# Optimization experiments

Hardware: AMD Instinct MI355X
Metric: run time of the kernel (lower is better)

The kernel has to match this reference:

```python
import jax, jax.numpy as jnp
from jax import lax
import numpy as np

DN = ('NCHW', 'OIHW', 'NCHW')

def conv(x, w, b, stride, pad):
    y = lax.conv_general_dilated(x, w, (stride, stride), [(pad, pad), (pad, pad)], dimension_numbers=DN)
    return y + b[None, :, None, None]

def conv_t(x, w, b, stride, pad):
    # PyTorch ConvTranspose2d weight layout is (in, out, kh, kw); flip spatially, swap to OIHW,
    # and realize transpose-conv as lhs-dilated conv with padding k-1-p.
    k = w.shape[2]
    wt = jnp.flip(w, (2, 3)).transpose(1, 0, 2, 3)
    q = k - 1 - pad
    y = lax.conv_general_dilated(x, wt, (1, 1), [(q, q), (q, q)], lhs_dilation=(stride, stride), dimension_numbers=DN)
    return y + b[None, :, None, None]

def setup_inputs() -> dict:
    key = jax.random.key(0)
    ks = jax.random.split(key, 16)
    K, C = 512, 64
    def he(k, shape, fan_in):
        return jax.random.normal(k, shape, jnp.float32) * np.float32(np.sqrt(2.0 / fan_in))
    return {
        'x': jax.random.normal(ks[0], (64, 1, 256, 256), jnp.float32),
        'e1_w': he(ks[1], (32, 1, 4, 4), 1 * 16), 'e1_b': jnp.zeros((32,), jnp.float32),
        'e2_w': he(ks[2], (64, 32, 4, 4), 32 * 16), 'e2_b': jnp.zeros((64,), jnp.float32),
        'e3_w': he(ks[3], (64, 64, 3, 3), 64 * 9), 'e3_b': jnp.zeros((64,), jnp.float32),
        'emb': jax.random.uniform(ks[4], (K, C), jnp.float32, -1.0 / K, 1.0 / K),
        'd1_w': he(ks[5], (64, 32, 3, 3), 64 * 9), 'd1_b': jnp.zeros((32,), jnp.float32),
        'd2_w': he(ks[6], (32, 64, 4, 4), 32 * 16), 'd2_b': jnp.zeros((64,), jnp.float32),
        'd3_w': he(ks[7], (64, 1, 4, 4), 64 * 16), 'd3_b': jnp.zeros((1,), jnp.float32),
    }

def reference(x, e1_w, e1_b, e2_w, e2_b, e3_w, e3_b, emb, d1_w, d1_b, d2_w, d2_b, d3_w, d3_b):
    # encoder
    h = jax.nn.relu(conv(x, e1_w, e1_b, 2, 1))
    h = jax.nn.relu(conv(h, e2_w, e2_b, 2, 1))
    ze = jax.nn.relu(conv(h, e3_w, e3_b, 1, 1))  # (N, C, H, W)
    N, C, H, W = ze.shape
    # VQ: nearest codebook entry per spatial location via ||z||^2 - 2 z.e + ||e||^2
    zf = ze.transpose(0, 2, 3, 1).reshape(-1, C)  # (N*H*W, C)
    dist = (zf * zf).sum(-1, keepdims=True) - 2.0 * (zf @ emb.T) + (emb * emb).sum(-1)[None, :]
    idx = jnp.argmin(dist, axis=1)  # (N*H*W,)
    zq = emb[idx].reshape(N, H, W, C).transpose(0, 3, 1, 2)  # (N, C, H, W)
    # straight-through estimator
    dec_in = ze + lax.stop_gradient(zq - ze)
    # decoder
    h = jax.nn.relu(conv_t(dec_in, d1_w, d1_b, 1, 1))
    h = jax.nn.relu(conv_t(h, d2_w, d2_b, 2, 1))
    x_hat = conv_t(h, d3_w, d3_b, 2, 1)
    return (x_hat, ze, zq)
```

## Files before the change

kernel.cpp:

```cpp
#include <hip/hip_runtime.h>

typedef short short8 __attribute__((ext_vector_type(8)));
typedef float f32x4 __attribute__((ext_vector_type(4)));

union U8 { short8 s8; unsigned int u[4]; };

__device__ __forceinline__ unsigned short f2bf(float f) {
    unsigned int u = __float_as_uint(f);
    u = (u + 0x7fffu + ((u >> 16) & 1u)) >> 16;
    return (unsigned short)u;
}
__device__ __forceinline__ float bf2f(unsigned short s) {
    return __uint_as_float(((unsigned int)s) << 16);
}


__global__ __launch_bounds__(256) void k_e1i(
    const float* __restrict__ x, const float* __restrict__ e1w, const float* __restrict__ e1b,
    unsigned short* __restrict__ h1p2, unsigned int* __restrict__ ws_dw,
    const float* __restrict__ e2w, const float* __restrict__ e3w,
    const float* __restrict__ d1w, const float* __restrict__ d2w,
    const float* __restrict__ d3w, const float* __restrict__ emb,
    unsigned short* __restrict__ ape2, unsigned short* __restrict__ ape3,
    unsigned short* __restrict__ apd1, unsigned short* __restrict__ apd2,
    unsigned short* __restrict__ apd3, unsigned short* __restrict__ embbf,
    float* __restrict__ hninit)
{
    int bid = blockIdx.x;
    if (bid < 4096) {
        int idx = bid * 256 + threadIdx.x;
        int ow = idx & 127, oh = (idx >> 7) & 127, n = idx >> 14;
        const float* xn = x + (size_t)n * 65536;
        float patch[16];
#pragma unroll
        for (int kh = 0; kh < 4; kh++) {
            int ih = 2 * oh + kh - 1;
#pragma unroll
            for (int kw = 0; kw < 4; kw++) {
                int iw = 2 * ow + kw - 1;
                bool ok = ((unsigned)ih < 256u) & ((unsigned)iw < 256u);
                patch[kh * 4 + kw] = ok ? xn[ih * 256 + iw] : 0.f;
            }
        }
        unsigned int outw[16];
#pragma unroll
        for (int oc = 0; oc < 32; oc++) {
            float acc = e1b[oc];
#pragma unroll
            for (int t = 0; t < 16; t++) acc += patch[t] * e1w[oc * 16 + t];
            unsigned short bf = f2bf(fmaxf(acc, 0.f));
            if (oc & 1) outw[oc >> 1] |= ((unsigned int)bf) << 16;
            else        outw[oc >> 1] = bf;
        }
        int par = ow & 1;
        int cidx = (ow + par) >> 1;
        size_t base = ((size_t)((idx >> 14) * 130 + oh + 1) * 2 + par) * 2112 + cidx * 32;
        uint4* dst = (uint4*)(h1p2 + base);
#pragma unroll
        for (int i = 0; i < 4; i++) dst[i] = *(uint4*)&outw[i * 4];
        return;
    }
    if (bid < 11376) {
        int t = (bid - 4096) * 256 + threadIdx.x;
        if (t < 270336) {
            int img = t / 4224, q = t % 4224;
            int rowsel = q / 2112, rem = q % 2112;
            ws_dw[img * 274560 + rowsel * 129 * 2112 + rem] = 0u;
        } else if (t < 532480) {
            int g = t - 270336;
            int img = g / 4096, q = g % 4096;
            int row = 1 + (q >> 5), c2 = q & 31;
            int sel = c2 >> 4, ch = c2 & 15;
            int par = sel ? 0 : 1, idx2 = sel ? 64 : 0;
            ws_dw[img * 274560 + row * 2112 + par * 1056 + idx2 * 16 + ch] = 0u;
        } else if (t < 1863680) {
            unsigned int base, Cd, r;
            if (t < 1064960)      { base = 17571840u; Cd = 32; r = t - 532480;  }
            else if (t < 1597440) { base = 34881536u; Cd = 32; r = t - 1064960; }
            else                  { base = 43802624u; Cd = 16; r = t - 1597440; }
            unsigned int per_img = 260u * Cd;
            unsigned int img = r / per_img, q = r % per_img;
            unsigned int p = q / Cd, c = q % Cd;
            unsigned int row, col;
            if (p < 66u)        { row = 0;  col = p; }
            else if (p < 132u)  { row = 65; col = p - 66u; }
            else { unsigned int s = p - 132u; row = 1 + (s >> 1); col = (s & 1) ? 65u : 0u; }
            ws_dw[base + ((img * 66u + row) * 66u + col) * Cd + c] = 0u;
        }
        return;
    }
    int f = (bid - 11376) * 256 + threadIdx.x;
    if (f < 4096) {
        int ks = f >> 8, mt = (f >> 6) & 3, lane = f & 63;
        int quad = lane >> 4, l16 = lane & 15;
        int oc = mt * 16 + l16, kh = ks >> 2, kw = ks & 3;
        short8 sv;
#pragma unroll
        for (int j = 0; j < 8; j++) {
            int ic = quad * 8 + j;
            sv[j] = (short)f2bf(e2w[((oc * 32 + ic) * 4 + kh) * 4 + kw]);
        }
        ((short8*)ape2)[f] = sv;
    } else if (f < 8704) {
        int g = f - 4096;
        int ks = g >> 8, mt = (g >> 6) & 3, lane = g & 63;
        int quad = lane >> 4, l16 = lane & 15;
        int oc = mt * 16 + l16, tap = ks >> 1, kh = tap / 3, kw = tap % 3;
        int icb = (ks & 1) * 32 + quad * 8;
        short8 sv;
#pragma unroll
        for (int j = 0; j < 8; j++)
            sv[j] = (short)f2bf(e3w[((oc * 64 + icb + j) * 3 + kh) * 3 + kw]);
        ((short8*)ape3)[g] = sv;
    } else if (f < 11008) {
        int g = f - 8704;
        int ks = g >> 7, mt = (g >> 6) & 1, lane = g & 63;
        int quad = lane >> 4, l16 = lane & 15;
        int oc = mt * 16 + l16, tap = ks >> 1, kh = tap / 3, kw = tap % 3;
        int icb = (ks & 1) * 32 + quad * 8;
        short8 sv;
#pragma unroll
        for (int j = 0; j < 8; j++)
            sv[j] = (short)f2bf(d1w[(((icb + j) * 32 + oc) * 3 + (2 - kh)) * 3 + (2 - kw)]);
        ((short8*)apd1)[g] = sv;
    } else if (f < 15104) {
        int g = f - 11008;
        int par = g >> 10, ks = (g >> 8) & 3, mt = (g >> 6) & 3, lane = g & 63;
        int quad = lane >> 4, l16 = lane & 15;
        int ph = par >> 1, pw = par & 1, a = ks >> 1, bb = ks & 1;
        int kh = 3 - ph - 2 * a, kw = 3 - pw - 2 * bb;
        int oc = mt * 16 + l16;
        short8 sv;
#pragma unroll
        for (int j = 0; j < 8; j++) {
            int ic = quad * 8 + j;
            sv[j] = (short)f2bf(d2w[((ic * 64 + oc) * 4 + kh) * 4 + kw]);
        }
        ((short8*)apd2)[g] = sv;
    } else if (f < 15232) {
        int g = f - 15104;
        int ks = g >> 6, lane = g & 63;
        int quad = lane >> 4, tap = lane & 15;
        short8 sv;
#pragma unroll
        for (int j = 0; j < 8; j++) {
            int ic = ks * 32 + quad * 8 + j;
            sv[j] = (short)f2bf(d3w[ic * 16 + tap]);
        }
        ((short8*)apd3)[g] = sv;
    } else if (f < 19328) {
        int g = f - 15232;
        int code = g >> 3, chb = (g & 7) * 8;
        short8 sv;
#pragma unroll
        for (int j = 0; j < 8; j++) sv[j] = (short)f2bf(emb[code * 64 + chb + j]);
        ((short8*)embbf)[g] = sv;
    } else if (f < 19840) {
        int code = f - 19328;
        float s = 0.f;
        for (int c = 0; c < 64; c++) { float v = emb[code * 64 + c]; s += v * v; }
        hninit[code] = 2.0f - 0.5f * s;
    }
}

template<int CIN, int COUT, int KSTEPS, int NCH, int WPIN, int MODE>
__global__ __launch_bounds__(256, 4) void k_conv(const unsigned short* __restrict__ inp,
                                                 const unsigned short* __restrict__ aprep,
                                                 const float* __restrict__ bias,
                                                 unsigned short* __restrict__ out0) {
    constexpr int MT = COUT / 16;
    constexpr int KCH = KSTEPS / NCH;
    __shared__ short8 sA[KCH * MT * 64];
    int tid = threadIdx.x;
    int wave = tid >> 6, lane = tid & 63, quad = lane >> 4, l16 = lane & 15;
    int bid = blockIdx.x;
    int n = bid >> 4, rg = bid & 15;
    int oh = rg * 4 + wave;

    int base0;
    if (MODE == 0) base0 = (n * 130 + 2 * oh) * 4224 + quad * 8;
    else           base0 = n * (WPIN * WPIN * CIN) + ((oh + 1) * WPIN + 1) * CIN + quad * 8;

    f32x4 acc[4][MT];
#pragma unroll
    for (int t = 0; t < 4; t++)
#pragma unroll
        for (int mt = 0; mt < MT; mt++)
            acc[t][mt] = *(const f32x4*)(bias + mt * 16 + quad * 4);

#pragma unroll
    for (int ch = 0; ch < NCH; ch++) {
        for (int i = tid; i < KCH * MT * 64; i += 256)
            sA[i] = ((const short8*)aprep)[ch * (KCH * MT * 64) + i];
        __syncthreads();
#pragma unroll
        for (int k = 0; k < KCH; k++) {
            int ks = ch * KCH + k;
            int off, pxs;
            if (MODE == 0) {
                int kh = ks >> 2, kw = ks & 3;
                int par = (kw & 1) ^ 1;
                off = kh * 4224 + par * 2112 + (kw >> 1) * 32;
                pxs = 32;
            } else {
                int tap = ks >> 1, kh = tap / 3, kw = tap % 3;
                off = ((kh - 1) * WPIN + (kw - 1)) * CIN + (ks & 1) * 32;
                pxs = CIN;
            }
            short8 bfr[4];
#pragma unroll
            for (int t = 0; t < 4; t++)
                bfr[t] = *(const short8*)(inp + base0 + (t * 16 + l16) * pxs + off);
#pragma unroll
            for (int mt = 0; mt < MT; mt++) {
                short8 a = sA[(k * MT + mt) * 64 + lane];
#pragma unroll
                for (int t = 0; t < 4; t++)
                    acc[t][mt] = __builtin_amdgcn_mfma_f32_16x16x32_bf16(a, bfr[t], acc[t][mt], 0, 0, 0);
            }
        }
        if (ch + 1 < NCH) __syncthreads();
    }

#pragma unroll
    for (int t = 0; t < 4; t++) {
        int ow = t * 16 + l16;
#pragma unroll
        for (int mt = 0; mt < MT; mt++) {
            float v0 = fmaxf(acc[t][mt][0], 0.f), v1 = fmaxf(acc[t][mt][1], 0.f);
            float v2 = fmaxf(acc[t][mt][2], 0.f), v3 = fmaxf(acc[t][mt][3], 0.f);
            unsigned int lo = (unsigned int)f2bf(v0) | ((unsigned int)f2bf(v1) << 16);
            unsigned int hi = (unsigned int)f2bf(v2) | ((unsigned int)f2bf(v3) << 16);
            uint2 uu; uu.x = lo; uu.y = hi;
            int oc = mt * 16 + quad * 4;
            if (MODE == 0) {
                size_t addr = (size_t)n * 278784 + ((oh + 1) * 66 + ow + 1) * 64 + oc;
                *(uint2*)(out0 + addr) = uu;
            } else {
                size_t addr = (size_t)n * 139392 + ((oh + 1) * 66 + ow + 1) * 32 + oc;
                *(uint2*)(out0 + addr) = uu;
            }
        }
    }
}

__global__ __launch_bounds__(256, 4) void k_e3vq(const unsigned short* __restrict__ h2p,
                                                 const unsigned short* __restrict__ ape3,
                                                 const float* __restrict__ bias,
                                                 const unsigned short* __restrict__ embbf,
                                                 const float* __restrict__ hninit,
                                                 float* __restrict__ ze_out,
                                                 float* __restrict__ zq_out,
                                                 unsigned short* __restrict__ zqp) {
    __shared__ short8 sA[9 * 4 * 64];
    int tid = threadIdx.x;
    int wave = tid >> 6, lane = tid & 63, quad = lane >> 4, l16 = lane & 15;
    int bid = blockIdx.x;
    int n = bid >> 4, rg = bid & 15;
    int oh = rg * 4 + wave;
    int base0 = n * 278784 + ((oh + 1) * 66 + 1) * 64 + quad * 8;

    f32x4 acc[4][4];
#pragma unroll
    for (int t = 0; t < 4; t++)
#pragma unroll
        for (int mt = 0; mt < 4; mt++)
            acc[t][mt] = *(const f32x4*)(bias + mt * 16 + quad * 4);

#pragma unroll
    for (int ch = 0; ch < 2; ch++) {
        for (int i = tid; i < 9 * 4 * 64; i += 256)
            sA[i] = ((const short8*)ape3)[ch * (9 * 4 * 64) + i];
        __syncthreads();
#pragma unroll
        for (int k = 0; k < 9; k++) {
            int ks = ch * 9 + k;
            int tap = ks >> 1, kh = tap / 3, kw = tap % 3;
            int off = ((kh - 1) * 66 + (kw - 1)) * 64 + (ks & 1) * 32;
            short8 bfr[4];
#pragma unroll
            for (int t = 0; t < 4; t++)
                bfr[t] = *(const short8*)(h2p + base0 + (t * 16 + l16) * 64 + off);
#pragma unroll
            for (int mt = 0; mt < 4; mt++) {
                short8 a = sA[(k * 4 + mt) * 64 + lane];
#pragma unroll
                for (int t = 0; t < 4; t++)
                    acc[t][mt] = __builtin_amdgcn_mfma_f32_16x16x32_bf16(a, bfr[t], acc[t][mt], 0, 0, 0);
            }
        }
        if (ch == 0) __syncthreads();
    }

#pragma unroll
    for (int t = 0; t < 4; t++)
#pragma unroll
        for (int mt = 0; mt < 4; mt++)
#pragma unroll
            for (int r = 0; r < 4; r++)
                acc[t][mt][r] = fmaxf(acc[t][mt][r], 0.f);

#pragma unroll
    for (int t = 0; t < 4; t++) {
        int px = oh * 64 + t * 16 + l16;
#pragma unroll
        for (int mt = 0; mt < 4; mt++) {
            int oc = mt * 16 + quad * 4;
#pragma unroll
            for (int r = 0; r < 4; r++)
                __builtin_nontemporal_store(acc[t][mt][r], &ze_out[((size_t)n * 64 + oc + r) * 4096 + px]);
        }
    }

    short8 b0[4], b1[4];
    int s0 = (((2 * quad) & 3) << 4) | l16;
    int s1 = (((2 * quad + 1) & 3) << 4) | l16;
#pragma unroll
    for (int t = 0; t < 4; t++) {
        f32x4 xv = (quad < 2) ? acc[t][0] : acc[t][1];
        f32x4 yv = (quad < 2) ? acc[t][2] : acc[t][3];
        unsigned int xa = (unsigned int)f2bf(xv[0]) | ((unsigned int)f2bf(xv[1]) << 16);
        unsigned int xb = (unsigned int)f2bf(xv[2]) | ((unsigned int)f2bf(xv[3]) << 16);
        unsigned int ya = (unsigned int)f2bf(yv[0]) | ((unsigned int)f2bf(yv[1]) << 16);
        unsigned int yb = (unsigned int)f2bf(yv[2]) | ((unsigned int)f2bf(yv[3]) << 16);
        U8 ub0, ub1;
        ub0.u[0] = (unsigned int)__shfl((int)xa, s0); ub0.u[1] = (unsigned int)__shfl((int)xb, s0);
        ub0.u[2] = (unsigned int)__shfl((int)xa, s1); ub0.u[3] = (unsigned int)__shfl((int)xb, s1);
        ub1.u[0] = (unsigned int)__shfl((int)ya, s0); ub1.u[1] = (unsigned int)__shfl((int)yb, s0);
        ub1.u[2] = (unsigned int)__shfl((int)ya, s1); ub1.u[3] = (unsigned int)__shfl((int)yb, s1);
        b0[t] = ub0.s8; b1[t] = ub1.s8;
    }

    unsigned int bk[4] = {0u, 0u, 0u, 0u};
#pragma unroll 4
    for (int j0 = 0; j0 < 512; j0 += 16) {
        short8 a0 = *(const short8*)(embbf + (j0 + l16) * 64 + quad * 8);
        short8 a1 = *(const short8*)(embbf + (j0 + l16) * 64 + 32 + quad * 8);
        f32x4 ci = *(const f32x4*)(hninit + j0 + quad * 4);
        int iv = 511 - j0 - quad * 4;
#pragma unroll
        for (int t = 0; t < 4; t++) {
            f32x4 s = __builtin_amdgcn_mfma_f32_16x16x32_bf16(a0, b0[t], ci, 0, 0, 0);
            s = __builtin_amdgcn_mfma_f32_16x16x32_bf16(a1, b1[t], s, 0, 0, 0);
#pragma unroll
            for (int r = 0; r < 4; r++) {
                unsigned int key = (__float_as_uint(s[r]) & 0xFFFFFE00u) | (unsigned int)(iv - r);
                bk[t] = bk[t] > key ? bk[t] : key;
            }
        }
    }
#pragma unroll
    for (int t = 0; t < 4; t++) {
        unsigned int o1 = (unsigned int)__shfl_xor((int)bk[t], 16);
        bk[t] = bk[t] > o1 ? bk[t] : o1;
        unsigned int o2 = (unsigned int)__shfl_xor((int)bk[t], 32);
        bk[t] = bk[t] > o2 ? bk[t] : o2;
    }
#pragma unroll
    for (int t = 0; t < 4; t++) {
        int code = 511 - (int)(bk[t] & 511u);
        int col = t * 16 + l16;
        int hw = oh * 64 + col;
        uint4 u0 = *(const uint4*)(embbf + code * 64 + quad * 16);
        uint4 u1 = *(const uint4*)(embbf + code * 64 + quad * 16 + 8);
        size_t qaddr = (size_t)n * 278784 + ((oh + 1) * 66 + (col + 1)) * 64 + quad * 16;
        *(uint4*)(zqp + qaddr) = u0;
        *(uint4*)(zqp + qaddr + 8) = u1;
        size_t zb = ((size_t)n * 64 + quad * 16) * 4096 + hw;
        unsigned int uw[8] = {u0.x, u0.y, u0.z, u0.w, u1.x, u1.y, u1.z, u1.w};
#pragma unroll
        for (int i = 0; i < 8; i++) {
            __builtin_nontemporal_store(__uint_as_float(uw[i] << 16), &zq_out[zb + (2 * i + 0) * 4096]);
            __builtin_nontemporal_store(__uint_as_float(uw[i] & 0xFFFF0000u), &zq_out[zb + (2 * i + 1) * 4096]);
        }
    }
}

__global__ __launch_bounds__(256, 3) void k_d2f(const unsigned short* __restrict__ d1op,
                                                const unsigned short* __restrict__ apd2,
                                                const float* __restrict__ bias,
                                                const unsigned short* __restrict__ apd3,
                                                unsigned short* __restrict__ sc16) {
    __shared__ short8 sA[1024];
    int tid = threadIdx.x;
    int wave = tid >> 6, lane = tid & 63, quad = lane >> 4, l16 = lane & 15;
    int bid = blockIdx.x;
    int n = bid >> 6, par = (bid >> 4) & 3, rg = bid & 15;
    int oh = rg * 4 + wave;
    int ph = par >> 1, pw = par & 1;

    short8 pa0 = ((const short8*)apd3)[lane];
    short8 pa1 = ((const short8*)apd3)[64 + lane];

    for (int i = tid; i < 1024; i += 256) sA[i] = ((const short8*)apd2)[par * 1024 + i];
    __syncthreads();

    int base0 = n * 139392 + ((oh + ph) * 66 + pw) * 32 + quad * 8;
    f32x4 acc[4][4];
#pragma unroll
    for (int t = 0; t < 4; t++)
#pragma unroll
        for (int mt = 0; mt < 4; mt++)
            acc[t][mt] = *(const f32x4*)(bias + mt * 16 + quad * 4);

#pragma unroll
    for (int k = 0; k < 4; k++) {
        int a_ = k >> 1, bb = k & 1;
        int off = (a_ * 66 + bb) * 32;
        short8 bfr[4];
#pragma unroll
        for (int t = 0; t < 4; t++)
            bfr[t] = *(const short8*)(d1op + base0 + (t * 16 + l16) * 32 + off);
#pragma unroll
        for (int mt = 0; mt < 4; mt++) {
            short8 a = sA[(k * 4 + mt) * 64 + lane];
#pragma unroll
            for (int t = 0; t < 4; t++)
                acc[t][mt] = __builtin_amdgcn_mfma_f32_16x16x32_bf16(a, bfr[t], acc[t][mt], 0, 0, 0);
        }
    }

    int s0 = (((2 * quad) & 3) << 4) | l16;
    int s1 = (((2 * quad + 1) & 3) << 4) | l16;
    int oh_out = 2 * oh + ph;
#pragma unroll
    for (int t = 0; t < 4; t++) {
#pragma unroll
        for (int mt = 0; mt < 4; mt++)
#pragma unroll
            for (int r = 0; r < 4; r++)
                acc[t][mt][r] = fmaxf(acc[t][mt][r], 0.f);
        f32x4 xv = (quad < 2) ? acc[t][0] : acc[t][1];
        f32x4 yv = (quad < 2) ? acc[t][2] : acc[t][3];
        unsigned int xa = (unsigned int)f2bf(xv[0]) | ((unsigned int)f2bf(xv[1]) << 16);
        unsigned int xb = (unsigned int)f2bf(xv[2]) | ((unsigned int)f2bf(xv[3]) << 16);
        unsigned int ya = (unsigned int)f2bf(yv[0]) | ((unsigned int)f2bf(yv[1]) << 16);
        unsigned int yb = (unsigned int)f2bf(yv[2]) | ((unsigned int)f2bf(yv[3]) << 16);
        U8 ub0, ub1;
        ub0.u[0] = (unsigned int)__shfl((int)xa, s0); ub0.u[1] = (unsigned int)__shfl((int)xb, s0);
        ub0.u[2] = (unsigned int)__shfl((int)xa, s1); ub0.u[3] = (unsigned int)__shfl((int)xb, s1);
        ub1.u[0] = (unsigned int)__shfl((int)ya, s0); ub1.u[1] = (unsigned int)__shfl((int)yb, s0);
        ub1.u[2] = (unsigned int)__shfl((int)ya, s1); ub1.u[3] = (unsigned int)__shfl((int)yb, s1);
        f32x4 sc = {0.f, 0.f, 0.f, 0.f};
        sc = __builtin_amdgcn_mfma_f32_16x16x32_bf16(pa0, ub0.s8, sc, 0, 0, 0);
        sc = __builtin_amdgcn_mfma_f32_16x16x32_bf16(pa1, ub1.s8, sc, 0, 0, 0);
        int ow_out = 2 * (t * 16 + l16) + pw;
        int pbaseo = n * 16384 + oh_out * 128 + ow_out;
#pragma unroll
        for (int r = 0; r < 4; r++) {
            int tap = quad * 4 + r;
            sc16[(size_t)tap * 1048576 + pbaseo] = f2bf(sc[r]);
        }
    }
}

__global__ __launch_bounds__(256) void k_d3e(const unsigned short* __restrict__ sc16,
                                             const float* __restrict__ d3b,
                                             float* __restrict__ xhat) {
    int idx = blockIdx.x * 256 + threadIdx.x;
    int ow = idx & 255, oh = (idx >> 8) & 255, n = idx >> 16;
    float acc = d3b[0];
    int kh0 = (oh + 1) & 1, kw0 = (ow + 1) & 1;
#pragma unroll
    for (int dh = 0; dh < 2; dh++) {
        int kh = kh0 + 2 * dh;
        int ih = (oh + 1 - kh) >> 1;
        bool vh = ((unsigned)ih < 128u);
#pragma unroll
        for (int dw = 0; dw < 2; dw++) {
            int kw = kw0 + 2 * dw;
            int iw = (ow + 1 - kw) >> 1;
            if (vh && ((unsigned)iw < 128u))
                acc += bf2f(sc16[(size_t)(kh * 4 + kw) * 1048576 + n * 16384 + ih * 128 + iw]);
        }
    }
    __builtin_nontemporal_store(acc, &xhat[(size_t)n * 65536 + oh * 256 + ow]);
}

extern "C" void kernel_launch(void* const* d_in, const int* in_sizes, int n_in,
                              void* d_out, int out_size, void* d_ws, size_t ws_size,
                              hipStream_t stream) {
    const float* x    = (const float*)d_in[0];
    const float* e1w  = (const float*)d_in[1];
    const float* e1b  = (const float*)d_in[2];
    const float* e2w  = (const float*)d_in[3];
    const float* e2b  = (const float*)d_in[4];
    const float* e3w  = (const float*)d_in[5];
    const float* e3b  = (const float*)d_in[6];
    const float* emb  = (const float*)d_in[7];
    const float* d1w  = (const float*)d_in[8];
    const float* d1b  = (const float*)d_in[9];
    const float* d2w  = (const float*)d_in[10];
    const float* d2b  = (const float*)d_in[11];
    const float* d3w  = (const float*)d_in[12];
    const float* d3b  = (const float*)d_in[13];

    float* xhat = (float*)d_out;
    float* ze   = xhat + 4194304;
    float* zq   = ze + 16777216;

    char* ws = (char*)d_ws;
    unsigned short* h1p2   = (unsigned short*)(ws + 0);
    unsigned short* h2p    = (unsigned short*)(ws + 70287360);
    unsigned short* zqp    = (unsigned short*)(ws + 139526144);
    unsigned short* d1op   = (unsigned short*)(ws + 175210496);
    unsigned short* sc16   = (unsigned short*)(ws + 193052672);
    unsigned short* ape2   = (unsigned short*)(ws + 226607104);
    unsigned short* ape3   = (unsigned short*)(ws + 226672640);
    unsigned short* apd1   = (unsigned short*)(ws + 226746368);
    unsigned short* apd2   = (unsigned short*)(ws + 226783232);
    unsigned short* apd3   = (unsigned short*)(ws + 226848768);
    unsigned short* embbf  = (unsigned short*)(ws + 226850816);
    float*          hninit = (float*)(ws + 226916352);

    k_e1i<<<11454, 256, 0, stream>>>(x, e1w, e1b, h1p2, (unsigned int*)d_ws,
                                     e2w, e3w, d1w, d2w, d3w, emb,
                                     ape2, ape3, apd1, apd2, apd3, embbf, hninit);
    k_conv<32, 64, 16, 2, 0, 0><<<1024, 256, 0, stream>>>(h1p2, ape2, e2b, h2p);
    k_e3vq<<<1024, 256, 0, stream>>>(h2p, ape3, e3b, embbf, hninit, ze, zq, zqp);
    k_conv<64, 32, 18, 2, 66, 2><<<1024, 256, 0, stream>>>(zqp, apd1, d1b, d1op);
    k_d2f<<<4096, 256, 0, stream>>>(d1op, apd2, d2b, apd3, sc16);
    k_d3e<<<16384, 256, 0, stream>>>(sc16, d3b, xhat);
}
```

Measured before the change: 422.9 us.

## Split VQ codebook search across waves via shared-memory tiles and cross-wave argmax

```diff
diff --git a/kernel.cpp b/kernel.cpp
--- a/kernel.cpp
+++ b/kernel.cpp
@@ -252,7 +252,11 @@
                                                  float* __restrict__ ze_out,
                                                  float* __restrict__ zq_out,
                                                  unsigned short* __restrict__ zqp) {
-    __shared__ short8 sA[9 * 4 * 64];
+    __shared__ __align__(16) char smem[36864];
+    short8* sA = (short8*)smem;
+    short8* sB = (short8*)smem;
+    unsigned int* cross = (unsigned int*)(smem + 32768);
+
     int tid = threadIdx.x;
     int wave = tid >> 6, lane = tid & 63, quad = lane >> 4, l16 = lane & 15;
     int bid = blockIdx.x;
@@ -291,6 +295,7 @@
         }
         if (ch == 0) __syncthreads();
     }
+    __syncthreads();
 
 #pragma unroll
     for (int t = 0; t < 4; t++)
@@ -312,7 +317,6 @@
         }
     }
 
-    short8 b0[4], b1[4];
     int s0 = (((2 * quad) & 3) << 4) | l16;
     int s1 = (((2 * quad + 1) & 3) << 4) | l16;
 #pragma unroll
@@ -328,20 +332,28 @@
         ub0.u[2] = (unsigned int)__shfl((int)xa, s1); ub0.u[3] = (unsigned int)__shfl((int)xb, s1);
         ub1.u[0] = (unsigned int)__shfl((int)ya, s0); ub1.u[1] = (unsigned int)__shfl((int)yb, s0);
         ub1.u[2] = (unsigned int)__shfl((int)ya, s1); ub1.u[3] = (unsigned int)__shfl((int)yb, s1);
-        b0[t] = ub0.s8; b1[t] = ub1.s8;
-    }
-
-    unsigned int bk[4] = {0u, 0u, 0u, 0u};
-#pragma unroll 4
-    for (int j0 = 0; j0 < 512; j0 += 16) {
+        sB[(wave * 8 + 2 * t + 0) * 64 + lane] = ub0.s8;
+        sB[(wave * 8 + 2 * t + 1) * 64 + lane] = ub1.s8;
+    }
+    __syncthreads();
+
+    unsigned int bk[16];
+#pragma unroll
+    for (int t = 0; t < 16; t++) bk[t] = 0u;
+    int j0base = wave * 128;
+#pragma unroll 2
+    for (int jj = 0; jj < 8; jj++) {
+        int j0 = j0base + jj * 16;
         short8 a0 = *(const short8*)(embbf + (j0 + l16) * 64 + quad * 8);
         short8 a1 = *(const short8*)(embbf + (j0 + l16) * 64 + 32 + quad * 8);
         f32x4 ci = *(const f32x4*)(hninit + j0 + quad * 4);
         int iv = 511 - j0 - quad * 4;
 #pragma unroll
-        for (int t = 0; t < 4; t++) {
-            f32x4 s = __builtin_amdgcn_mfma_f32_16x16x32_bf16(a0, b0[t], ci, 0, 0, 0);
-            s = __builtin_amdgcn_mfma_f32_16x16x32_bf16(a1, b1[t], s, 0, 0, 0);
+        for (int t = 0; t < 16; t++) {
+            short8 vb0 = sB[(2 * t + 0) * 64 + lane];
+            short8 vb1 = sB[(2 * t + 1) * 64 + lane];
+            f32x4 s = __builtin_amdgcn_mfma_f32_16x16x32_bf16(a0, vb0, ci, 0, 0, 0);
+            s = __builtin_amdgcn_mfma_f32_16x16x32_bf16(a1, vb1, s, 0, 0, 0);
 #pragma unroll
             for (int r = 0; r < 4; r++) {
                 unsigned int key = (__float_as_uint(s[r]) & 0xFFFFFE00u) | (unsigned int)(iv - r);
@@ -350,16 +362,28 @@
         }
     }
 #pragma unroll
-    for (int t = 0; t < 4; t++) {
+    for (int t = 0; t < 16; t++) {
         unsigned int o1 = (unsigned int)__shfl_xor((int)bk[t], 16);
         bk[t] = bk[t] > o1 ? bk[t] : o1;
         unsigned int o2 = (unsigned int)__shfl_xor((int)bk[t], 32);
         bk[t] = bk[t] > o2 ? bk[t] : o2;
     }
-#pragma unroll
-    for (int t = 0; t < 4; t++) {
-        int code = 511 - (int)(bk[t] & 511u);
-        int col = t * 16 + l16;
+    if (quad == 0) {
+#pragma unroll
+        for (int t = 0; t < 16; t++)
+            cross[(t * 16 + l16) * 4 + wave] = bk[t];
+    }
+    __syncthreads();
+
+#pragma unroll
+    for (int j = 0; j < 4; j++) {
+        int tile = wave * 4 + j;
+        uint4 k4 = *(const uint4*)(cross + (tile * 16 + l16) * 4);
+        unsigned int key = k4.x > k4.y ? k4.x : k4.y;
+        unsigned int k2 = k4.z > k4.w ? k4.z : k4.w;
+        key = key > k2 ? key : k2;
+        int code = 511 - (int)(key & 511u);
+        int col = j * 16 + l16;
         int hw = oh * 64 + col;
         uint4 u0 = *(const uint4*)(embbf + code * 64 + quad * 16);
         uint4 u1 = *(const uint4*)(embbf + code * 64 + quad * 16 + 8);
@@ -376,7 +400,7 @@
     }
 }
 
-__global__ __launch_bounds__(256, 3) void k_d2f(const unsigned short* __restrict__ d1op,
+__global__ __launch_bounds__(256, 4) void k_d2f(const unsigned short* __restrict__ d1op,
                                                 const unsigned short* __restrict__ apd2,
                                                 const float* __restrict__ bias,
                                                 const unsigned short* __restrict__ apd3,
```

Result: slower. 511.8 us (+21.0%).
